# Kernel optimization log

Hardware: AMD Instinct MI355X
Metric: run time of the kernel (lower is better)

Reference implementation:

```python
import jax, jax.numpy as jnp
import numpy as np
import math

HEADS = 8
KSIZE = 25  # decomposition moving-average window

def moving_avg(x, k):
    # x: [B, S, E]; replicate-pad last axis by (k-1)//2 on both sides, window mean (stride 1)
    p = (k - 1) // 2
    xp = jnp.pad(x, ((0, 0), (0, 0), (p, p)), mode='edge')
    cs = jnp.cumsum(xp, axis=-1)
    cs = jnp.concatenate([jnp.zeros_like(cs[..., :1]), cs], axis=-1)
    return (cs[..., k:] - cs[..., :-k]) / k

def decompose(x, k):
    trend = moving_avg(x, k)
    return x - trend, trend

def setup_inputs() -> dict:
    key = jax.random.key(0)
    ks = jax.random.split(key, 16)
    B, S, E = 4, 2048, 256
    H = HEADS
    D = E // H
    FF = 4 * E
    OUT = E
    s = 0.02
    inp = {
        'x': jax.random.normal(ks[0], (B, S, E), dtype=jnp.float32),
        'mask': jnp.ones((B, 1, 1, S), dtype=jnp.int32),
        'wq': jax.random.normal(ks[1], (D, D), dtype=jnp.float32) * s,
        'wk': jax.random.normal(ks[2], (D, D), dtype=jnp.float32) * s,
        'wv': jax.random.normal(ks[3], (D, D), dtype=jnp.float32) * s,
        'w_out': jax.random.normal(ks[4], (E, E), dtype=jnp.float32) * s,
        'b_out': jnp.zeros((E,), dtype=jnp.float32),
        'ff_w1': jax.random.normal(ks[5], (E, FF), dtype=jnp.float32) * s,
        'ff_b1': jnp.zeros((FF,), dtype=jnp.float32),
        'ff_w2': jax.random.normal(ks[6], (FF, E), dtype=jnp.float32) * s,
        'ff_b2': jnp.zeros((E,), dtype=jnp.float32),
        'pr_w1': jax.random.normal(ks[7], (E, FF), dtype=jnp.float32) * s,
        'pr_b1': jnp.zeros((FF,), dtype=jnp.float32),
        'pr_w2': jax.random.normal(ks[8], (FF, OUT), dtype=jnp.float32) * s,
        'pr_b2': jnp.zeros((OUT,), dtype=jnp.float32),
    }
    return inp

def reference(x, mask, wq, wk, wv, w_out, b_out, ff_w1, ff_b1, ff_w2, ff_b2, pr_w1, pr_b1, pr_w2, pr_b2):
    B, S, E = x.shape
    H = HEADS
    D = E // H
    # multihead attention (per-head shared projections, scale by sqrt(embed_size))
    xh = x.reshape(B, S, H, D)
    q = xh @ wq
    k = xh @ wk
    v = xh @ wv
    scores = jnp.einsum('nqhd,nkhd->nhqk', q, k) / jnp.float32(math.sqrt(E))
    scores = jnp.where(mask == 0, jnp.float32(-1e20), scores)
    attn = jax.nn.softmax(scores, axis=-1)
    attn_out = jnp.einsum('nhqk,nkhd->nqhd', attn, v).reshape(B, S, E)
    attn_out = attn_out @ w_out + b_out
    # residual (dropout is identity at inference)
    x = x + attn_out
    # first decomposition: keep seasonal part
    y, _ = decompose(x, KSIZE)
    # FFN
    z = jnp.maximum(y @ ff_w1 + ff_b1, 0.0) @ ff_w2 + ff_b2
    s = y + z
    # second decomposition
    s, _ = decompose(s, KSIZE)
    # projection FFN
    out = jnp.maximum(s @ pr_w1 + pr_b1, 0.0) @ pr_w2 + pr_b2
    return out
```

## Files before the change

kernel.cpp:

```cpp
#include <hip/hip_runtime.h>
#include <hip/hip_bf16.h>
#include <math.h>

#define B_   4
#define S_   2048
#define E_   256
#define H_   8
#define D_   32
#define FF_  1024
#define NTOK (B_*S_)

typedef __attribute__((ext_vector_type(8))) short short8;
typedef __attribute__((ext_vector_type(4))) float f32x4;
typedef __attribute__((ext_vector_type(4))) unsigned u32x4;
typedef __hip_bfloat16 bf16;

#define QSCALE 0.09016844005556021f

__device__ __forceinline__ unsigned short round_bf16(float a) {
    unsigned ua = __builtin_bit_cast(unsigned, a);
    return (unsigned short)((ua + 0x7fffu + ((ua >> 16) & 1u)) >> 16);
}
__device__ __forceinline__ unsigned cvtpk_bf16(float lo, float hi) {
    unsigned r;
    asm("v_cvt_pk_bf16_f32 %0, %1, %2" : "=v"(r) : "v"(lo), "v"(hi));
    return r;
}
__device__ __forceinline__ float fexp2(float x) {
    float r;
    asm("v_exp_f32 %0, %1" : "=v"(r) : "v"(x));
    return r;
}
__device__ __forceinline__ void gld16(const short* g, short* l) {
    __builtin_amdgcn_global_load_lds(
        (const __attribute__((address_space(1))) unsigned int*)g,
        (__attribute__((address_space(3))) unsigned int*)l, 16, 0, 0);
}
__device__ __forceinline__ short8 lds_frag(const short* base, int r, int c16) {
    return *(const short8*)(base + r*64 + (((c16) ^ (r & 7)) << 3));
}

__global__ __launch_bounds__(256) void qkv_prep_kernel(
    const float* __restrict__ x,
    const float* __restrict__ wq, const float* __restrict__ wk, const float* __restrict__ wv,
    bf16* __restrict__ q, bf16* __restrict__ k, bf16* __restrict__ v,
    const float* __restrict__ w_out, const float* __restrict__ ff_w1,
    const float* __restrict__ ff_w2, const float* __restrict__ pr_w1,
    const float* __restrict__ pr_w2,
    unsigned short* __restrict__ woT, unsigned short* __restrict__ f1T,
    unsigned short* __restrict__ f2T, unsigned short* __restrict__ p1T,
    unsigned short* __restrict__ p2T,
    const int* __restrict__ mask, int* __restrict__ mflags)
{
    const int bid = blockIdx.x;
    if (bid >= 512) {
        const int pb = bid - 512;
        if (pb >= 1088) {
            const int t = threadIdx.x;
            if (t < 128) {
                const int* p = mask + (t >> 5)*S_ + (t & 31)*64;
                int any0 = 0;
                #pragma unroll
                for (int i = 0; i < 16; ++i) {
                    const int4 vv = *(const int4*)(p + i*4);
                    if (!(vv.x && vv.y && vv.z && vv.w)) any0 = 1;
                }
                mflags[t] = any0;
            }
            return;
        }
        const float* w; unsigned short* wt; int K, N, idx;
        if (pb < 64)       { w = w_out; wt = woT; K = E_;  N = E_;  idx = pb; }
        else if (pb < 320) { w = ff_w1; wt = f1T; K = E_;  N = FF_; idx = pb - 64; }
        else if (pb < 576) { w = ff_w2; wt = f2T; K = FF_; N = E_;  idx = pb - 320; }
        else if (pb < 832) { w = pr_w1; wt = p1T; K = E_;  N = FF_; idx = pb - 576; }
        else               { w = pr_w2; wt = p2T; K = FF_; N = E_;  idx = pb - 832; }
        const int nb = N/32;
        const int n0 = (idx % nb)*32, k0 = (idx / nb)*32;
        __shared__ float tile[32][33];
        const int c = threadIdx.x & 31, r0 = threadIdx.x >> 5;
        #pragma unroll
        for (int i = 0; i < 4; ++i)
            tile[r0 + 8*i][c] = w[(size_t)(k0 + r0 + 8*i)*N + n0 + c];
        __syncthreads();
        #pragma unroll
        for (int i = 0; i < 4; ++i)
            wt[(size_t)(n0 + r0 + 8*i)*K + k0 + c] = round_bf16(tile[c][r0 + 8*i]);
        return;
    }
    __shared__ float wqs[D_*D_], wks[D_*D_], wvs[D_*D_];
    __shared__ float xs[16][E_];
    const int tid = threadIdx.x;
    for (int i = tid; i < D_*D_; i += 256) {
        wqs[i] = wq[i]; wks[i] = wk[i]; wvs[i] = wv[i];
    }
    const int tok0 = bid * 16;
    #pragma unroll
    for (int i = 0; i < 16; ++i)
        xs[i][tid] = x[(size_t)(tok0 + i)*E_ + tid];
    __syncthreads();
    const int h = tid >> 5, d = tid & 31;
    for (int t = 0; t < 16; ++t) {
        float aq = 0.f, ak = 0.f, av = 0.f;
        #pragma unroll
        for (int i = 0; i < D_; ++i) {
            const float xv = xs[t][h*D_ + i];
            aq += xv * wqs[i*D_ + d];
            ak += xv * wks[i*D_ + d];
            av += xv * wvs[i*D_ + d];
        }
        const int tok = tok0 + t;
        const int b = tok >> 11;
        const int s = tok & (S_-1);
        const int u = s & 63;
        const int sp = (s & ~63) | (((u>>5)&1)*32 + ((u>>2)&1)*16 + ((u>>3)&3)*4 + (u&3));
        const size_t base = (size_t)(b*H_ + h)*S_;
        q[(base + s )*D_ + d] = __float2bfloat16(aq * QSCALE);
        k[(base + sp)*D_ + d] = __float2bfloat16(ak);
        v[(base + s )*D_ + d] = __float2bfloat16(av);
    }
}

__global__ __launch_bounds__(256) void vtrans_kernel(
    const short* __restrict__ v, short* __restrict__ vt)
{
    __shared__ short t2[D_][256];
    const int tid = threadIdx.x;
    const int bh = blockIdx.x >> 3;
    const int s0 = (blockIdx.x & 7) * 256;
    const short* src = v + ((size_t)bh*S_ + s0 + tid)*D_;
    const short8 r0 = *(const short8*)(src);
    const short8 r1 = *(const short8*)(src + 8);
    const short8 r2 = *(const short8*)(src + 16);
    const short8 r3 = *(const short8*)(src + 24);
    #pragma unroll
    for (int i = 0; i < 8; ++i) {
        t2[i     ][tid] = r0[i];
        t2[i + 8 ][tid] = r1[i];
        t2[i + 16][tid] = r2[i];
        t2[i + 24][tid] = r3[i];
    }
    __syncthreads();
    const int d = tid >> 3, j = tid & 7;
    short* dst = vt + ((size_t)(bh*D_ + d))*S_ + s0 + j*32;
    const short8* row = (const short8*)&t2[d][j*32];
    const short8 o0 = row[0], o1 = row[1], o2 = row[2], o3 = row[3];
    *(short8*)(dst     ) = o0;
    *(short8*)(dst + 8 ) = o1;
    *(short8*)(dst + 16) = o2;
    *(short8*)(dst + 24) = o3;
}

__global__ __launch_bounds__(256) void attn_mfma_kernel(
    const short* __restrict__ qg, const short* __restrict__ kg,
    const short* __restrict__ vtg, const int* __restrict__ mask,
    const int* __restrict__ mflags, unsigned short* __restrict__ attn_out)
{
    __shared__ alignas(16) short lk[2][64*32];
    __shared__ alignas(16) short lv[2][32*64];

    const int tid  = threadIdx.x;
    const int lane = tid & 63;
    const int wid  = tid >> 6;
    const int c    = lane & 15;
    const int g    = lane >> 4;
    const int p    = ((int)blockIdx.x & 7)*64 + ((int)blockIdx.x >> 3);
    const int bh   = p >> 4;
    const int qt   = p & 15;
    const int b    = bh >> 3;
    const int h    = bh & 7;
    const int q0   = qt*128 + wid*32;

    const short* qrow = qg + ((size_t)bh*S_ + q0 + c)*D_ + g*8;
    const short8 qfA = *(const short8*)(qrow);
    const short8 qfB = *(const short8*)(qrow + 16*D_);
    const short* kbase = kg  + (size_t)bh*S_*D_;
    const short* vbase = vtg + (size_t)bh*D_*S_;
    const int*   mrow  = mask + b*S_;

    const int fl = (lane < 32) ? mflags[b*32 + lane] : 0;
    const unsigned long long mbits = __ballot(fl != 0);

    const short* sbase; int soff0, soff1, sinc, dchunk0;
    if (wid < 2) {
        const int R0 = wid*32 + (lane >> 2);
        const int R1 = R0 + 16;
        const int s  = lane & 3;
        soff0 = R0*D_ + ((s ^ ((R0 >> 1) & 3)) << 3);
        soff1 = R1*D_ + ((s ^ ((R1 >> 1) & 3)) << 3);
        sbase = kbase; sinc = 64*D_;
        dchunk0 = wid*1024;
    } else {
        const int r0 = (wid - 2)*16 + (lane >> 3);
        const int r1 = r0 + 8;
        const int s  = lane & 7;
        soff0 = r0*S_ + ((s ^ (r0 & 7)) << 3);
        soff1 = r1*S_ + ((s ^ (r1 & 7)) << 3);
        sbase = vbase; sinc = 64;
        dchunk0 = (wid - 2)*1024;
    }

    const int kaddr = c*D_ + ((g ^ ((c >> 1) & 3)) << 3);
    const int va0   = c*64 + ((g       ^ (c & 7)) << 3);
    const int va1   = c*64 + (((g + 4) ^ (c & 7)) << 3);
    const f32x4 zero = {0.f,0.f,0.f,0.f};
    const short8 ones = { (short)0x3F80, (short)0x3F80, (short)0x3F80, (short)0x3F80,
                          (short)0x3F80, (short)0x3F80, (short)0x3F80, (short)0x3F80 };
    f32x4 oA0 = zero, oA1 = zero, oB0 = zero, oB1 = zero;
    f32x4 lAacc = zero, lBacc = zero;

    {
        short* d0 = (wid < 2 ? &lk[0][0] : &lv[0][0]) + dchunk0;
        gld16(sbase + soff0, d0);
        gld16(sbase + soff1, d0 + 512);
    }
    __syncthreads();

    int buf = 0;
    for (int t = 0; t < 32; ++t) {
        if (t < 31) {
            const short* sp = sbase + (size_t)(t + 1)*sinc;
            short* d0 = (wid < 2 ? &lk[buf ^ 1][0] : &lv[buf ^ 1][0]) + dchunk0;
            gld16(sp + soff0, d0);
            gld16(sp + soff1, d0 + 512);
        }
        const short* LK = &lk[buf][0];
        const short* LV = &lv[buf][0];
        const short8 kf0 = *(const short8*)(LK + kaddr);
        const short8 kf1 = *(const short8*)(LK + kaddr + 512);
        const short8 kf2 = *(const short8*)(LK + kaddr + 1024);
        const short8 kf3 = *(const short8*)(LK + kaddr + 1536);
        __builtin_amdgcn_s_setprio(1);
        f32x4 sA0 = __builtin_amdgcn_mfma_f32_16x16x32_bf16(kf0, qfA, zero, 0, 0, 0);
        f32x4 sA1 = __builtin_amdgcn_mfma_f32_16x16x32_bf16(kf1, qfA, zero, 0, 0, 0);
        f32x4 sA2 = __builtin_amdgcn_mfma_f32_16x16x32_bf16(kf2, qfA, zero, 0, 0, 0);
        f32x4 sA3 = __builtin_amdgcn_mfma_f32_16x16x32_bf16(kf3, qfA, zero, 0, 0, 0);
        f32x4 sB0 = __builtin_amdgcn_mfma_f32_16x16x32_bf16(kf0, qfB, zero, 0, 0, 0);
        f32x4 sB1 = __builtin_amdgcn_mfma_f32_16x16x32_bf16(kf1, qfB, zero, 0, 0, 0);
        f32x4 sB2 = __builtin_amdgcn_mfma_f32_16x16x32_bf16(kf2, qfB, zero, 0, 0, 0);
        f32x4 sB3 = __builtin_amdgcn_mfma_f32_16x16x32_bf16(kf3, qfB, zero, 0, 0, 0);
        __builtin_amdgcn_s_setprio(0);
        if ((mbits >> t) & 1ull) {
            const int kb = t*64 + 8*g;
            #pragma unroll
            for (int r = 0; r < 4; ++r) {
                if (mrow[kb      + r] == 0) { sA0[r] = -1e20f; sB0[r] = -1e20f; }
                if (mrow[kb + 4  + r] == 0) { sA1[r] = -1e20f; sB1[r] = -1e20f; }
                if (mrow[kb + 32 + r] == 0) { sA2[r] = -1e20f; sB2[r] = -1e20f; }
                if (mrow[kb + 36 + r] == 0) { sA3[r] = -1e20f; sB3[r] = -1e20f; }
            }
        }
        f32x4 pA0, pA1, pA2, pA3, pB0, pB1, pB2, pB3;
        #pragma unroll
        for (int r = 0; r < 4; ++r) {
            pA0[r] = fexp2(sA0[r]); pA1[r] = fexp2(sA1[r]);
            pA2[r] = fexp2(sA2[r]); pA3[r] = fexp2(sA3[r]);
            pB0[r] = fexp2(sB0[r]); pB1[r] = fexp2(sB1[r]);
            pB2[r] = fexp2(sB2[r]); pB3[r] = fexp2(sB3[r]);
        }
        const short8 pafA0 = __builtin_bit_cast(short8,
            (u32x4){ cvtpk_bf16(pA0[0],pA0[1]), cvtpk_bf16(pA0[2],pA0[3]),
                     cvtpk_bf16(pA1[0],pA1[1]), cvtpk_bf16(pA1[2],pA1[3]) });
        const short8 pafA1 = __builtin_bit_cast(short8,
            (u32x4){ cvtpk_bf16(pA2[0],pA2[1]), cvtpk_bf16(pA2[2],pA2[3]),
                     cvtpk_bf16(pA3[0],pA3[1]), cvtpk_bf16(pA3[2],pA3[3]) });
        const short8 pafB0 = __builtin_bit_cast(short8,
            (u32x4){ cvtpk_bf16(pB0[0],pB0[1]), cvtpk_bf16(pB0[2],pB0[3]),
                     cvtpk_bf16(pB1[0],pB1[1]), cvtpk_bf16(pB1[2],pB1[3]) });
        const short8 pafB1 = __builtin_bit_cast(short8,
            (u32x4){ cvtpk_bf16(pB2[0],pB2[1]), cvtpk_bf16(pB2[2],pB2[3]),
                     cvtpk_bf16(pB3[0],pB3[1]), cvtpk_bf16(pB3[2],pB3[3]) });
        const short8 vf0 = *(const short8*)(LV + va0);
        const short8 vf1 = *(const short8*)(LV + va1);
        const short8 vf2 = *(const short8*)(LV + va0 + 1024);
        const short8 vf3 = *(const short8*)(LV + va1 + 1024);
        __builtin_amdgcn_s_setprio(1);
        oA0 = __builtin_amdgcn_mfma_f32_16x16x32_bf16(vf0, pafA0, oA0, 0, 0, 0);
        oA0 = __builtin_amdgcn_mfma_f32_16x16x32_bf16(vf1, pafA1, oA0, 0, 0, 0);
        oA1 = __builtin_amdgcn_mfma_f32_16x16x32_bf16(vf2, pafA0, oA1, 0, 0, 0);
        oA1 = __builtin_amdgcn_mfma_f32_16x16x32_bf16(vf3, pafA1, oA1, 0, 0, 0);
        oB0 = __builtin_amdgcn_mfma_f32_16x16x32_bf16(vf0, pafB0, oB0, 0, 0, 0);
        oB0 = __builtin_amdgcn_mfma_f32_16x16x32_bf16(vf1, pafB1, oB0, 0, 0, 0);
        oB1 = __builtin_amdgcn_mfma_f32_16x16x32_bf16(vf2, pafB0, oB1, 0, 0, 0);
        oB1 = __builtin_amdgcn_mfma_f32_16x16x32_bf16(vf3, pafB1, oB1, 0, 0, 0);
        lAacc = __builtin_amdgcn_mfma_f32_16x16x32_bf16(ones, pafA0, lAacc, 0, 0, 0);
        lAacc = __builtin_amdgcn_mfma_f32_16x16x32_bf16(ones, pafA1, lAacc, 0, 0, 0);
        lBacc = __builtin_amdgcn_mfma_f32_16x16x32_bf16(ones, pafB0, lBacc, 0, 0, 0);
        lBacc = __builtin_amdgcn_mfma_f32_16x16x32_bf16(ones, pafB1, lBacc, 0, 0, 0);
        __builtin_amdgcn_s_setprio(0);
        __syncthreads();
        buf ^= 1;
    }
    const float invA = 1.0f / lAacc[0], invB = 1.0f / lBacc[0];
    unsigned short* orowA = attn_out + ((size_t)b*S_ + q0 + c)*E_ + h*D_ + g*4;
    unsigned short* orowB = orowA + (size_t)16*E_;
    uint2 a0, a1, b0, b1;
    a0.x = cvtpk_bf16(oA0[0]*invA, oA0[1]*invA); a0.y = cvtpk_bf16(oA0[2]*invA, oA0[3]*invA);
    a1.x = cvtpk_bf16(oA1[0]*invA, oA1[1]*invA); a1.y = cvtpk_bf16(oA1[2]*invA, oA1[3]*invA);
    b0.x = cvtpk_bf16(oB0[0]*invB, oB0[1]*invB); b0.y = cvtpk_bf16(oB0[2]*invB, oB0[3]*invB);
    b1.x = cvtpk_bf16(oB1[0]*invB, oB1[1]*invB); b1.y = cvtpk_bf16(oB1[2]*invB, oB1[3]*invB);
    *(uint2*)(orowA)      = a0;
    *(uint2*)(orowA + 16) = a1;
    *(uint2*)(orowB)      = b0;
    *(uint2*)(orowB + 16) = b1;
}

template<int BM, int BN, int DB, int RELU, int RESID, int WF32, int WBF16>
__global__ __launch_bounds__(256) void mgemm_kernel(
    const short* __restrict__ A, const short* __restrict__ WT,
    const float* __restrict__ bias, const float* __restrict__ R,
    float* __restrict__ C32, unsigned short* __restrict__ Cb,
    int M, int N, int K)
{
    constexpr int FR = BM / 32;
    constexpr int FC = BN / 32;
    constexpr int NB = DB ? 2 : 1;
    __shared__ alignas(16) short As[NB][BM*64];
    __shared__ alignas(16) short Bs[NB][BN*64];
    const int t = threadIdx.x, w = t >> 6, lane = t & 63;
    const int col = lane & 15, grp = lane >> 4;
    const int wm = w >> 1, wn = w & 1;
    const int gx = N / BN;
    const int nwg = gridDim.x;
    const int lin = ((int)blockIdx.x & 7)*(nwg >> 3) + ((int)blockIdx.x >> 3);
    const int bm = lin / gx, bn = lin % gx;
    const int arow = t >> 3, ac = t & 7;

    f32x4 acc[FR][FC];
    #pragma unroll
    for (int i = 0; i < FR; ++i)
        #pragma unroll
        for (int j = 0; j < FC; ++j) acc[i][j] = (f32x4){0.f,0.f,0.f,0.f};

    if (DB) {
        #pragma unroll
        for (int b2 = 0; b2 < BM/32; ++b2) {
            const int row = b2*32 + arow;
            gld16(A + (size_t)(bm*BM + row)*K + ((ac ^ (row & 7)) << 3),
                  &As[0][0] + b2*2048 + w*512);
        }
        #pragma unroll
        for (int b2 = 0; b2 < BN/32; ++b2) {
            const int row = b2*32 + arow;
            gld16(WT + (size_t)(bn*BN + row)*K + ((ac ^ (row & 7)) << 3),
                  &Bs[0][0] + b2*2048 + w*512);
        }
        __syncthreads();
        int buf = 0;
        for (int kb = 0; kb < K; kb += 64) {
            if (kb + 64 < K) {
                #pragma unroll
                for (int b2 = 0; b2 < BM/32; ++b2) {
                    const int row = b2*32 + arow;
                    gld16(A + (size_t)(bm*BM + row)*K + kb + 64 + ((ac ^ (row & 7)) << 3),
                          &As[buf ^ 1][0] + b2*2048 + w*512);
                }
                #pragma unroll
                for (int b2 = 0; b2 < BN/32; ++b2) {
                    const int row = b2*32 + arow;
                    gld16(WT + (size_t)(bn*BN + row)*K + kb + 64 + ((ac ^ (row & 7)) << 3),
                          &Bs[buf ^ 1][0] + b2*2048 + w*512);
                }
            }
            #pragma unroll
            for (int s = 0; s < 2; ++s) {
                short8 af[FR], bf_[FC];
                #pragma unroll
                for (int fr = 0; fr < FR; ++fr)
                    af[fr] = lds_frag(&As[buf][0], wm*(BM/2) + fr*16 + col, s*4 + grp);
                #pragma unroll
                for (int fc = 0; fc < FC; ++fc)
                    bf_[fc] = lds_frag(&Bs[buf][0], wn*(BN/2) + fc*16 + col, s*4 + grp);
                #pragma unroll
                for (int fr = 0; fr < FR; ++fr)
                    #pragma unroll
                    for (int fc = 0; fc < FC; ++fc)
                        acc[fr][fc] = __builtin_amdgcn_mfma_f32_16x16x32_bf16(af[fr], bf_[fc], acc[fr][fc], 0, 0, 0);
            }
            __syncthreads();
            buf ^= 1;
        }
    } else {
        for (int kb = 0; kb < K; kb += 64) {
            #pragma unroll
            for (int b2 = 0; b2 < BM/32; ++b2) {
                const int row = b2*32 + arow;
                gld16(A + (size_t)(bm*BM + row)*K + kb + ((ac ^ (row & 7)) << 3),
                      &As[0][0] + b2*2048 + w*512);
            }
            #pragma unroll
            for (int b2 = 0; b2 < BN/32; ++b2) {
                const int row = b2*32 + arow;
                gld16(WT + (size_t)(bn*BN + row)*K + kb + ((ac ^ (row & 7)) << 3),
                      &Bs[0][0] + b2*2048 + w*512);
            }
            __syncthreads();
            #pragma unroll
            for (int s = 0; s < 2; ++s) {
                short8 af[FR], bf_[FC];
                #pragma unroll
                for (int fr = 0; fr < FR; ++fr)
                    af[fr] = lds_frag(&As[0][0], wm*(BM/2) + fr*16 + col, s*4 + grp);
                #pragma unroll
                for (int fc = 0; fc < FC; ++fc)
                    bf_[fc] = lds_frag(&Bs[0][0], wn*(BN/2) + fc*16 + col, s*4 + grp);
                #pragma unroll
                for (int fr = 0; fr < FR; ++fr)
                    #pragma unroll
                    for (int fc = 0; fc < FC; ++fc)
                        acc[fr][fc] = __builtin_amdgcn_mfma_f32_16x16x32_bf16(af[fr], bf_[fc], acc[fr][fc], 0, 0, 0);
            }
            __syncthreads();
        }
    }

    #pragma unroll
    for (int fc = 0; fc < FC; ++fc) {
        const int n = bn*BN + wn*(BN/2) + fc*16 + col;
        const float bs = bias[n];
        #pragma unroll
        for (int fr = 0; fr < FR; ++fr) {
            #pragma unroll
            for (int reg = 0; reg < 4; ++reg) {
                const int m = bm*BM + wm*(BM/2) + fr*16 + grp*4 + reg;
                float v = acc[fr][fc][reg] + bs;
                if (RELU) v = fmaxf(v, 0.f);
                if (RESID) v += R[(size_t)m*N + n];
                if (WF32) C32[(size_t)m*N + n] = v;
                if (WBF16) Cb[(size_t)m*N + n] = round_bf16(v);
            }
        }
    }
}

template<int WF32, int WBF16>
__global__ __launch_bounds__(256) void decomp_kernel(
    const float* __restrict__ in, float* __restrict__ o32, unsigned short* __restrict__ ob)
{
    __shared__ float r[E_];
    const int row = blockIdx.x, e = threadIdx.x;
    const float xv = in[(size_t)row*E_ + e];
    r[e] = xv;
    __syncthreads();
    float sum = 0.f;
    #pragma unroll
    for (int j = -12; j <= 12; ++j) {
        int idx = e + j;
        idx = idx < 0 ? 0 : (idx > E_-1 ? E_-1 : idx);
        sum += r[idx];
    }
    const float res = xv - sum * (1.0f/25.0f);
    if (WF32) o32[(size_t)row*E_ + e] = res;
    if (WBF16) ob[(size_t)row*E_ + e] = round_bf16(res);
}

extern "C" void kernel_launch(void* const* d_in, const int* in_sizes, int n_in,
                              void* d_out, int out_size, void* d_ws, size_t ws_size,
                              hipStream_t stream) {
    const float* x     = (const float*)d_in[0];
    const int*   mask  = (const int*)  d_in[1];
    const float* wq    = (const float*)d_in[2];
    const float* wk    = (const float*)d_in[3];
    const float* wv    = (const float*)d_in[4];
    const float* w_out = (const float*)d_in[5];
    const float* b_out = (const float*)d_in[6];
    const float* ff_w1 = (const float*)d_in[7];
    const float* ff_b1 = (const float*)d_in[8];
    const float* ff_w2 = (const float*)d_in[9];
    const float* ff_b2 = (const float*)d_in[10];
    const float* pr_w1 = (const float*)d_in[11];
    const float* pr_b1 = (const float*)d_in[12];
    const float* pr_w2 = (const float*)d_in[13];
    const float* pr_b2 = (const float*)d_in[14];
    float* out = (float*)d_out;

    char* ws = (char*)d_ws;
    const size_t MB = 1024ull*1024ull;
    const size_t KB = 1024ull;
    bf16*  qb    = (bf16*)(ws + 0*MB);
    bf16*  kbf   = (bf16*)(ws + 4*MB);
    bf16*  vbf   = (bf16*)(ws + 8*MB);
    bf16*  vtb   = (bf16*)(ws + 12*MB);
    unsigned short* attnb = (unsigned short*)(ws + 16*MB);
    float* x1    = (float*)(ws + 20*MB);
    float* y32   = (float*)(ws + 28*MB);
    unsigned short* yb  = (unsigned short*)(ws + 36*MB);
    unsigned short* h1  = (unsigned short*)(ws + 0*MB);
    float* s32   = (float*)(ws + 20*MB);
    unsigned short* s2b = (unsigned short*)(ws + 16*MB);
    unsigned short* h2  = (unsigned short*)(ws + 0*MB);
    unsigned short* woT = (unsigned short*)(ws + 40*MB);
    unsigned short* f1T = (unsigned short*)(ws + 40*MB + 128*KB);
    unsigned short* f2T = (unsigned short*)(ws + 40*MB + 640*KB);
    unsigned short* p1T = (unsigned short*)(ws + 40*MB + 1152*KB);
    unsigned short* p2T = (unsigned short*)(ws + 40*MB + 1664*KB);
    int*            mfl = (int*)           (ws + 40*MB + 2176*KB);

    qkv_prep_kernel<<<1601, 256, 0, stream>>>(x, wq, wk, wv, qb, kbf, vbf,
                                              w_out, ff_w1, ff_w2, pr_w1, pr_w2,
                                              woT, f1T, f2T, p1T, p2T, mask, mfl);
    vtrans_kernel<<<B_*H_*(S_/256), 256, 0, stream>>>((const short*)vbf, (short*)vtb);
    attn_mfma_kernel<<<B_*H_*S_/128, 256, 0, stream>>>(
        (const short*)qb, (const short*)kbf, (const short*)vtb, mask, mfl, attnb);
    mgemm_kernel<64,64,1,0,1,1,0><<<(NTOK/64)*(E_/64), 256, 0, stream>>>(
        (const short*)attnb, (const short*)woT, b_out, x, x1, nullptr, NTOK, E_, E_);
    decomp_kernel<1,1><<<NTOK, 256, 0, stream>>>(x1, y32, yb);
    mgemm_kernel<128,128,0,1,0,0,1><<<(NTOK/128)*(FF_/128), 256, 0, stream>>>(
        (const short*)yb, (const short*)f1T, ff_b1, nullptr, nullptr, h1, NTOK, FF_, E_);
    mgemm_kernel<64,64,1,0,1,1,0><<<(NTOK/64)*(E_/64), 256, 0, stream>>>(
        (const short*)h1, (const short*)f2T, ff_b2, y32, s32, nullptr, NTOK, E_, FF_);
    decomp_kernel<0,1><<<NTOK, 256, 0, stream>>>(s32, nullptr, s2b);
    mgemm_kernel<128,128,0,1,0,0,1><<<(NTOK/128)*(FF_/128), 256, 0, stream>>>(
        (const short*)s2b, (const short*)p1T, pr_b1, nullptr, nullptr, h2, NTOK, FF_, E_);
    mgemm_kernel<64,64,1,0,0,1,0><<<(NTOK/64)*(E_/64), 256, 0, stream>>>(
        (const short*)h2, (const short*)p2T, pr_b2, nullptr, out, nullptr, NTOK, E_, FF_);
}
```

Before: 126.1 us.

## Fuse decomposition into N=256 GEMMs and fold V transpose into QKV prep

```diff
diff --git a/kernel.cpp b/kernel.cpp
--- a/kernel.cpp
+++ b/kernel.cpp
@@ -43,7 +43,7 @@
 __global__ __launch_bounds__(256) void qkv_prep_kernel(
     const float* __restrict__ x,
     const float* __restrict__ wq, const float* __restrict__ wk, const float* __restrict__ wv,
-    bf16* __restrict__ q, bf16* __restrict__ k, bf16* __restrict__ v,
+    bf16* __restrict__ q, bf16* __restrict__ k, unsigned short* __restrict__ vt,
     const float* __restrict__ w_out, const float* __restrict__ ff_w1,
     const float* __restrict__ ff_w2, const float* __restrict__ pr_w1,
     const float* __restrict__ pr_w2,
@@ -90,6 +90,7 @@
     }
     __shared__ float wqs[D_*D_], wks[D_*D_], wvs[D_*D_];
     __shared__ float xs[16][E_];
+    __shared__ unsigned short vsh[16*256];
     const int tid = threadIdx.x;
     for (int i = tid; i < D_*D_; i += 256) {
         wqs[i] = wq[i]; wks[i] = wk[i]; wvs[i] = wv[i];
@@ -100,6 +101,8 @@
         xs[i][tid] = x[(size_t)(tok0 + i)*E_ + tid];
     __syncthreads();
     const int h = tid >> 5, d = tid & 31;
+    const int b  = tok0 >> 11;
+    const int s0 = tok0 & (S_-1);
     for (int t = 0; t < 16; ++t) {
         float aq = 0.f, ak = 0.f, av = 0.f;
         #pragma unroll
@@ -109,46 +112,25 @@
             ak += xv * wks[i*D_ + d];
             av += xv * wvs[i*D_ + d];
         }
-        const int tok = tok0 + t;
-        const int b = tok >> 11;
-        const int s = tok & (S_-1);
+        const int s = s0 + t;
         const int u = s & 63;
         const int sp = (s & ~63) | (((u>>5)&1)*32 + ((u>>2)&1)*16 + ((u>>3)&3)*4 + (u&3));
         const size_t base = (size_t)(b*H_ + h)*S_;
         q[(base + s )*D_ + d] = __float2bfloat16(aq * QSCALE);
         k[(base + sp)*D_ + d] = __float2bfloat16(ak);
-        v[(base + s )*D_ + d] = __float2bfloat16(av);
-    }
-}
-
-__global__ __launch_bounds__(256) void vtrans_kernel(
-    const short* __restrict__ v, short* __restrict__ vt)
-{
-    __shared__ short t2[D_][256];
-    const int tid = threadIdx.x;
-    const int bh = blockIdx.x >> 3;
-    const int s0 = (blockIdx.x & 7) * 256;
-    const short* src = v + ((size_t)bh*S_ + s0 + tid)*D_;
-    const short8 r0 = *(const short8*)(src);
-    const short8 r1 = *(const short8*)(src + 8);
-    const short8 r2 = *(const short8*)(src + 16);
-    const short8 r3 = *(const short8*)(src + 24);
+        vsh[t*256 + tid] = round_bf16(av);
+    }
+    __syncthreads();
+    unsigned vv[8];
     #pragma unroll
     for (int i = 0; i < 8; ++i) {
-        t2[i     ][tid] = r0[i];
-        t2[i + 8 ][tid] = r1[i];
-        t2[i + 16][tid] = r2[i];
-        t2[i + 24][tid] = r3[i];
-    }
-    __syncthreads();
-    const int d = tid >> 3, j = tid & 7;
-    short* dst = vt + ((size_t)(bh*D_ + d))*S_ + s0 + j*32;
-    const short8* row = (const short8*)&t2[d][j*32];
-    const short8 o0 = row[0], o1 = row[1], o2 = row[2], o3 = row[3];
-    *(short8*)(dst     ) = o0;
-    *(short8*)(dst + 8 ) = o1;
-    *(short8*)(dst + 16) = o2;
-    *(short8*)(dst + 24) = o3;
+        const unsigned lo = vsh[(2*i    )*256 + tid];
+        const unsigned hi = vsh[(2*i + 1)*256 + tid];
+        vv[i] = lo | (hi << 16);
+    }
+    unsigned short* dst = vt + ((size_t)((b*H_ + h)*D_ + d))*S_ + s0;
+    *(u32x4*)(dst)     = (u32x4){vv[0], vv[1], vv[2], vv[3]};
+    *(u32x4*)(dst + 8) = (u32x4){vv[4], vv[5], vv[6], vv[7]};
 }
 
 __global__ __launch_bounds__(256) void attn_mfma_kernel(
@@ -305,6 +287,117 @@
     *(uint2*)(orowB + 16) = b1;
 }
 
+template<int WF32, int WBF16>
+__global__ __launch_bounds__(256) void mgemm_dec_kernel(
+    const short* __restrict__ A, const short* __restrict__ WT,
+    const float* __restrict__ bias, const float* __restrict__ R,
+    float* __restrict__ o32, unsigned short* __restrict__ ob,
+    int M, int K)
+{
+    __shared__ alignas(16) short stage[2][18432];
+    float* dec = (float*)&stage[0][0];
+    const int t = threadIdx.x, w = t >> 6, lane = t & 63;
+    const int col = lane & 15, grp = lane >> 4;
+    const int wm = w >> 1, wn = w & 1;
+    const int nwg = gridDim.x;
+    const int bm = ((int)blockIdx.x & 7)*(nwg >> 3) + ((int)blockIdx.x >> 3);
+    const int arow = t >> 3, ac = t & 7;
+
+    f32x4 acc[8];
+    #pragma unroll
+    for (int j = 0; j < 8; ++j) acc[j] = (f32x4){0.f,0.f,0.f,0.f};
+
+    {
+        const int row = arow;
+        gld16(A + (size_t)(bm*32 + row)*K + ((ac ^ (row & 7)) << 3),
+              &stage[0][0] + w*512);
+        #pragma unroll
+        for (int b2 = 0; b2 < 8; ++b2) {
+            const int rowb = b2*32 + arow;
+            gld16(WT + (size_t)rowb*K + ((ac ^ (rowb & 7)) << 3),
+                  &stage[0][2048] + b2*2048 + w*512);
+        }
+    }
+    __syncthreads();
+
+    int buf = 0;
+    for (int kb = 0; kb < K; kb += 64) {
+        if (kb + 64 < K) {
+            const int row = arow;
+            gld16(A + (size_t)(bm*32 + row)*K + kb + 64 + ((ac ^ (row & 7)) << 3),
+                  &stage[buf ^ 1][0] + w*512);
+            #pragma unroll
+            for (int b2 = 0; b2 < 8; ++b2) {
+                const int rowb = b2*32 + arow;
+                gld16(WT + (size_t)rowb*K + kb + 64 + ((ac ^ (rowb & 7)) << 3),
+                      &stage[buf ^ 1][2048] + b2*2048 + w*512);
+            }
+        }
+        const short* As_ = &stage[buf][0];
+        const short* Bs_ = &stage[buf][2048];
+        #pragma unroll
+        for (int s = 0; s < 2; ++s) {
+            const short8 af = lds_frag(As_, wm*16 + col, s*4 + grp);
+            #pragma unroll
+            for (int fc = 0; fc < 8; ++fc) {
+                const short8 bf_ = lds_frag(Bs_, wn*128 + fc*16 + col, s*4 + grp);
+                acc[fc] = __builtin_amdgcn_mfma_f32_16x16x32_bf16(af, bf_, acc[fc], 0, 0, 0);
+            }
+        }
+        __syncthreads();
+        buf ^= 1;
+    }
+
+    #pragma unroll
+    for (int fc = 0; fc < 8; ++fc) {
+        const int n = wn*128 + fc*16 + col;
+        const float bs = bias[n];
+        #pragma unroll
+        for (int reg = 0; reg < 4; ++reg) {
+            const int m = wm*16 + grp*4 + reg;
+            float v = acc[fc][reg] + bs;
+            v += R[(size_t)(bm*32 + m)*E_ + n];
+            dec[m*261 + n] = v;
+        }
+    }
+    __syncthreads();
+    const int row = t & 31, ch = t >> 5;
+    const int c0 = ch * 32;
+    const float* dr = dec + row*261;
+    float sum = 0.f;
+    #pragma unroll
+    for (int j = -12; j <= 12; ++j) {
+        int jj = c0 + j;
+        jj = jj < 0 ? 0 : (jj > 255 ? 255 : jj);
+        sum += dr[jj];
+    }
+    float res[32];
+    #pragma unroll
+    for (int i = 0; i < 32; ++i) {
+        const int cc = c0 + i;
+        res[i] = dr[cc] - sum * (1.0f/25.0f);
+        const int hi = cc + 13 > 255 ? 255 : cc + 13;
+        const int lo = cc - 12 < 0 ? 0 : cc - 12;
+        sum += dr[hi] - dr[lo];
+    }
+    const size_t gro = (size_t)(bm*32 + row)*E_ + c0;
+    if (WF32) {
+        #pragma unroll
+        for (int i = 0; i < 8; ++i)
+            *(f32x4*)(o32 + gro + i*4) = (f32x4){res[4*i], res[4*i+1], res[4*i+2], res[4*i+3]};
+    }
+    if (WBF16) {
+        #pragma unroll
+        for (int i = 0; i < 4; ++i) {
+            u32x4 pk;
+            #pragma unroll
+            for (int j = 0; j < 4; ++j)
+                pk[j] = cvtpk_bf16(res[8*i + 2*j], res[8*i + 2*j + 1]);
+            *(u32x4*)(ob + gro + i*8) = pk;
+        }
+    }
+}
+
 template<int BM, int BN, int DB, int RELU, int RESID, int WF32, int WBF16>
 __global__ __launch_bounds__(256) void mgemm_kernel(
     const short* __restrict__ A, const short* __restrict__ WT,
@@ -433,27 +526,6 @@
     }
 }
 
-template<int WF32, int WBF16>
-__global__ __launch_bounds__(256) void decomp_kernel(
-    const float* __restrict__ in, float* __restrict__ o32, unsigned short* __restrict__ ob)
-{
-    __shared__ float r[E_];
-    const int row = blockIdx.x, e = threadIdx.x;
-    const float xv = in[(size_t)row*E_ + e];
-    r[e] = xv;
-    __syncthreads();
-    float sum = 0.f;
-    #pragma unroll
-    for (int j = -12; j <= 12; ++j) {
-        int idx = e + j;
-        idx = idx < 0 ? 0 : (idx > E_-1 ? E_-1 : idx);
-        sum += r[idx];
-    }
-    const float res = xv - sum * (1.0f/25.0f);
-    if (WF32) o32[(size_t)row*E_ + e] = res;
-    if (WBF16) ob[(size_t)row*E_ + e] = round_bf16(res);
-}
-
 extern "C" void kernel_launch(void* const* d_in, const int* in_sizes, int n_in,
                               void* d_out, int out_size, void* d_ws, size_t ws_size,
                               hipStream_t stream) {
@@ -479,14 +551,11 @@
     const size_t KB = 1024ull;
     bf16*  qb    = (bf16*)(ws + 0*MB);
     bf16*  kbf   = (bf16*)(ws + 4*MB);
-    bf16*  vbf   = (bf16*)(ws + 8*MB);
     bf16*  vtb   = (bf16*)(ws + 12*MB);
     unsigned short* attnb = (unsigned short*)(ws + 16*MB);
-    float* x1    = (float*)(ws + 20*MB);
     float* y32   = (float*)(ws + 28*MB);
     unsigned short* yb  = (unsigned short*)(ws + 36*MB);
     unsigned short* h1  = (unsigned short*)(ws + 0*MB);
-    float* s32   = (float*)(ws + 20*MB);
     unsigned short* s2b = (unsigned short*)(ws + 16*MB);
     unsigned short* h2  = (unsigned short*)(ws + 0*MB);
     unsigned short* woT = (unsigned short*)(ws + 40*MB);
@@ -496,20 +565,18 @@
     unsigned short* p2T = (unsigned short*)(ws + 40*MB + 1664*KB);
     int*            mfl = (int*)           (ws + 40*MB + 2176*KB);
 
-    qkv_prep_kernel<<<1601, 256, 0, stream>>>(x, wq, wk, wv, qb, kbf, vbf,
+    qkv_prep_kernel<<<1601, 256, 0, stream>>>(x, wq, wk, wv, qb, kbf,
+                                              (unsigned short*)vtb,
                                               w_out, ff_w1, ff_w2, pr_w1, pr_w2,
                                               woT, f1T, f2T, p1T, p2T, mask, mfl);
-    vtrans_kernel<<<B_*H_*(S_/256), 256, 0, stream>>>((const short*)vbf, (short*)vtb);
     attn_mfma_kernel<<<B_*H_*S_/128, 256, 0, stream>>>(
         (const short*)qb, (const short*)kbf, (const short*)vtb, mask, mfl, attnb);
-    mgemm_kernel<64,64,1,0,1,1,0><<<(NTOK/64)*(E_/64), 256, 0, stream>>>(
-        (const short*)attnb, (const short*)woT, b_out, x, x1, nullptr, NTOK, E_, E_);
-    decomp_kernel<1,1><<<NTOK, 256, 0, stream>>>(x1, y32, yb);
+    mgemm_dec_kernel<1,1><<<NTOK/32, 256, 0, stream>>>(
+        (const short*)attnb, (const short*)woT, b_out, x, y32, yb, NTOK, E_);
     mgemm_kernel<128,128,0,1,0,0,1><<<(NTOK/128)*(FF_/128), 256, 0, stream>>>(
         (const short*)yb, (const short*)f1T, ff_b1, nullptr, nullptr, h1, NTOK, FF_, E_);
-    mgemm_kernel<64,64,1,0,1,1,0><<<(NTOK/64)*(E_/64), 256, 0, stream>>>(
-        (const short*)h1, (const short*)f2T, ff_b2, y32, s32, nullptr, NTOK, E_, FF_);
-    decomp_kernel<0,1><<<NTOK, 256, 0, stream>>>(s32, nullptr, s2b);
+    mgemm_dec_kernel<0,1><<<NTOK/32, 256, 0, stream>>>(
+        (const short*)h1, (const short*)f2T, ff_b2, y32, nullptr, s2b, NTOK, FF_);
     mgemm_kernel<128,128,0,1,0,0,1><<<(NTOK/128)*(FF_/128), 256, 0, stream>>>(
         (const short*)s2b, (const short*)p1T, pr_b1, nullptr, nullptr, h2, NTOK, FF_, E_);
     mgemm_kernel<64,64,1,0,0,1,0><<<(NTOK/64)*(E_/64), 256, 0, stream>>>(
```

Result: faster. 120.0 us (-4.8%).
